# Performance work log

Hardware: AMD Instinct MI355X
Metric: run time of the kernel (lower is better)

Reference implementation:

```python
import jax, jax.numpy as jnp
import numpy as np

B, L, H, D = 4096, 256, 32, 2
LOG_PROB_FACTOR = 0.5

def setup_inputs() -> dict:
    key = jax.random.key(0)
    k0, k1, k2, k3 = jax.random.split(key, 4)
    x = jax.random.randint(k0, (B, L), 0, D)  # spin configs in {0,1}
    Wi = jax.random.normal(k1, (D, 4 * H), dtype=jnp.float32) * 0.1   # input kernel (no bias, flax LSTMCell)
    Wh = jax.random.normal(k2, (H, 4 * H), dtype=jnp.float32) * 0.1   # recurrent kernel
    bh = jnp.zeros((4 * H,), dtype=jnp.float32)                        # recurrent bias
    Wo = jax.random.normal(k3, (H, D), dtype=jnp.float32) * 0.1       # output Dense kernel
    bo = jnp.zeros((D,), dtype=jnp.float32)                            # output Dense bias
    return {"x": x, "Wi": Wi, "Wh": Wh, "bh": bh, "Wo": Wo, "bo": bo}

def reference(x, Wi, Wh, bh, Wo, bo):
    # one-hot of spin t-1 (zeros at t=0); log-prob is read out at spin t.
    x_oh = jax.nn.one_hot(x, D, dtype=Wi.dtype)      # [B, L, D]
    xs = jnp.swapaxes(x_oh, 0, 1)                    # [L, B, D] time-major for scan
    c0 = jnp.zeros((x.shape[0], H), Wi.dtype)
    h0 = jnp.zeros((x.shape[0], H), Wi.dtype)
    inp0 = jnp.zeros((x.shape[0], D), Wi.dtype)      # jnp.zeros(inputDim) initial input

    def step(carry, xt):
        c, h, inp = carry
        gates = inp @ Wi + h @ Wh + bh               # [B, 4H]
        i, f, g, o = jnp.split(gates, 4, axis=-1)    # flax LSTMCell gate order i,f,g,o
        c_new = jax.nn.sigmoid(f) * c + jax.nn.sigmoid(i) * jnp.tanh(g)
        h_new = jax.nn.sigmoid(o) * jnp.tanh(c_new)
        out = jax.nn.elu(h_new @ Wo + bo)            # Dense + actFun, [B, D]
        # log(sum(softmax(out) * onehot)) == gathered log_softmax (stable form)
        logp = jnp.sum(jax.nn.log_softmax(out, axis=-1) * xt, axis=-1)  # [B]
        return (c_new, h_new, xt), logp

    _, logps = jax.lax.scan(step, (c0, h0, inp0), xs)  # logps: [L, B]
    return LOG_PROB_FACTOR * jnp.sum(logps, axis=0)    # [B]
```

## Files before the change

kernel.cpp:

```cpp
#include <hip/hip_runtime.h>


typedef __attribute__((ext_vector_type(8))) short bf16x8;
typedef __attribute__((ext_vector_type(4))) float f32x4;

#define LOG2E 1.4426950408889634f
#define LN2   0.6931471805599453f

__device__ __forceinline__ float fexp2(float x) { return __builtin_amdgcn_exp2f(x); }
__device__ __forceinline__ float flog2(float x) { return __builtin_amdgcn_logf(x); }
__device__ __forceinline__ float frcp(float x)  { return __builtin_amdgcn_rcpf(x); }

__device__ __forceinline__ float fsig(float x)   { return frcp(1.f + fexp2(-LOG2E * x)); }
__device__ __forceinline__ float ftanh_(float x) { return 1.f - 2.f * frcp(fexp2(2.f * LOG2E * x) + 1.f); }
__device__ __forceinline__ float felu(float x)   { return x > 0.f ? x : fexp2(LOG2E * x) - 1.f; }

__device__ __forceinline__ unsigned short f2bf(float f) {
    unsigned u = __builtin_bit_cast(unsigned, f);
    u = (u + 0x7FFFu + ((u >> 16) & 1u)) >> 16;
    return (unsigned short)u;
}

__device__ __forceinline__ unsigned cvtpk_bf16(float a, float b) {
    unsigned r;
    asm("v_cvt_pk_bf16_f32 %0, %1, %2" : "=v"(r) : "v"(a), "v"(b));
    return r;
}

constexpr int Bsz = 4096;

__global__ __launch_bounds__(256, 1) void lstm_r19(
    const int*   __restrict__ x,
    const float* __restrict__ Wi,
    const float* __restrict__ Wh,
    const float* __restrict__ bh,
    const float* __restrict__ Wo,
    const float* __restrict__ bo,
    float*       __restrict__ out)
{
    const int tid  = threadIdx.x;
    const int w    = tid >> 6;
    const int lane = tid & 63;
    const int m    = lane & 15;
    const int oct  = lane >> 4;
    const int b0   = blockIdx.x * 16;

    extern __shared__ char dynpad[];
    __shared__ char   spinT[16][260];
    __shared__ float2 Sbuf[256][16];
    __shared__ short  hbuf[2][16][40];
    __shared__ float  red[16][16];
    if (blockIdx.x == 0xFFFFFFFFu) dynpad[0] = 1;

    {
        const int bl  = tid >> 4;
        const int c16 = (tid & 15) * 16;
        const int4* src = reinterpret_cast<const int4*>(x + (b0 + bl) * 256 + c16);
#pragma unroll
        for (int q = 0; q < 4; ++q) {
            const int4 v = src[q];
            const int pk = (v.x & 1) | ((v.y & 1) << 8) | ((v.z & 1) << 16) | ((v.w & 1) << 24);
            *reinterpret_cast<int*>(&spinT[bl][c16 + 4 * q]) = pk;
        }
    }

    bf16x8 wfrag[2];
    {
        const int r = m & 3;
        const float gs = (r == 2) ? 2.f * LOG2E : -LOG2E;
#pragma unroll
        for (int T = 0; T < 2; ++T) {
            const int colg = 32 * r + 8 * w + 2 * (m >> 2) + T;
#pragma unroll
            for (int j = 0; j < 8; ++j)
                wfrag[T][j] = (short)f2bf(gs * Wh[(8 * oct + j) * 128 + colg]);
        }
    }
    bf16x8 wfragO;
#pragma unroll
    for (int j = 0; j < 8; ++j)
        wfragO[j] = (m < 2) ? (short)f2bf(Wo[(8 * oct + j) * 2 + m]) : (short)0;

    const int uA = 8 * w + 2 * oct;
    const int uB = uA + 1;
    float bv0A[4], bvdA[4], bv0B[4], bvdB[4];
#pragma unroll
    for (int r = 0; r < 4; ++r) {
        const float gs = (r == 2) ? 2.f * LOG2E : -LOG2E;
        const int cA = 32 * r + uA, cB = 32 * r + uB;
        bv0A[r] = gs * (bh[cA] + Wi[cA]); bvdA[r] = gs * (Wi[128 + cA] - Wi[cA]);
        bv0B[r] = gs * (bh[cB] + Wi[cB]); bvdB[r] = gs * (Wi[128 + cB] - Wi[cB]);
    }
    const float bo0 = bo[0], bo1 = bo[1];

    float cA = fsig(bh[uA]) * ftanh_(bh[64 + uA]);
    float cB = fsig(bh[uB]) * ftanh_(bh[64 + uB]);
    {
        const float hA = fsig(bh[96 + uA]) * ftanh_(cA);
        const float hB = fsig(bh[96 + uB]) * ftanh_(cB);
        *reinterpret_cast<int*>(&hbuf[0][m][uA]) = (int)cvtpk_bf16(hA, hB);
    }
    __syncthreads();

    const f32x4 zero4 = { 0.f, 0.f, 0.f, 0.f };

    auto cellup = [](const f32x4 a, float& cc) -> float {
        const float ei = fexp2(a[0]), ef = fexp2(a[1]);
        const float eg = fexp2(a[2]), eo = fexp2(a[3]);
        const float P = (1.f + ei) * (1.f + eg);
        const float Q = 1.f + ef;
        const float R = frcp(P * Q);
        cc = fmaf(P * R, cc, (eg - 1.f) * Q * R);
        const float ec = fexp2(2.f * LOG2E * cc);
        return (ec - 1.f) * frcp((1.f + eo) * (1.f + ec));
    };

    auto step = [&](const int t, const int rb, const int wb,
                    const float spf, const int hw) {
        const bf16x8 hfrag =
            *reinterpret_cast<const bf16x8*>(&hbuf[rb][m][8 * oct]);

        f32x4 cbA, cbB;
#pragma unroll
        for (int r = 0; r < 4; ++r) {
            cbA[r] = fmaf(spf, bvdA[r], bv0A[r]);
            cbB[r] = fmaf(spf, bvdB[r], bv0B[r]);
        }

        const f32x4 accA = __builtin_amdgcn_mfma_f32_16x16x32_bf16(wfrag[0], hfrag, cbA, 0, 0, 0);
        const f32x4 accB = __builtin_amdgcn_mfma_f32_16x16x32_bf16(wfrag[1], hfrag, cbB, 0, 0, 0);

        if (w == hw) {
            const f32x4 aO = __builtin_amdgcn_mfma_f32_16x16x32_bf16(wfragO, hfrag, zero4, 0, 0, 0);
            if (oct == 0) Sbuf[t - 1][m] = make_float2(aO[0], aO[1]);
        }

        const float hA = cellup(accA, cA);
        const float hB = cellup(accB, cB);
        *reinterpret_cast<int*>(&hbuf[wb][m][uA]) = (int)cvtpk_bf16(hA, hB);
        __syncthreads();
    };

    unsigned sp4 = *reinterpret_cast<const unsigned*>(&spinT[m][0]);
    for (int tb = 1; tb < 253; tb += 4) {
        const unsigned sp4n =
            *reinterpret_cast<const unsigned*>(&spinT[m][tb + 3]);
        step(tb,     0, 1, (float)(sp4 & 0xFFu),         0);
        step(tb + 1, 1, 0, (float)((sp4 >> 8) & 0xFFu),  1);
        step(tb + 2, 0, 1, (float)((sp4 >> 16) & 0xFFu), 2);
        step(tb + 3, 1, 0, (float)(sp4 >> 24),           3);
        sp4 = sp4n;
    }
    step(253, 0, 1, (float)(sp4 & 0xFFu),         0);
    step(254, 1, 0, (float)((sp4 >> 8) & 0xFFu),  1);
    step(255, 0, 1, (float)((sp4 >> 16) & 0xFFu), 2);

    if (w == 3) {
        const bf16x8 hfrag = *reinterpret_cast<const bf16x8*>(&hbuf[1][m][8 * oct]);
        const f32x4 aO = __builtin_amdgcn_mfma_f32_16x16x32_bf16(wfragO, hfrag, zero4, 0, 0, 0);
        if (oct == 0) Sbuf[255][m] = make_float2(aO[0], aO[1]);
    }
    __syncthreads();

    float lp = 0.f;
    {
        const int bpost = tid & 15;
        const int tc    = tid >> 4;
#pragma unroll
        for (int i = 0; i < 16; ++i) {
            const int t = tc * 16 + i;
            const float2 sv = Sbuf[t][bpost];
            const int sp = spinT[bpost][t];
            const float o0 = felu(sv.x + bo0);
            const float o1 = felu(sv.y + bo1);
            const float mx = fmaxf(o0, o1), mn = fminf(o0, o1);
            const float lse = mx + LN2 * flog2(1.f + fexp2(LOG2E * (mn - mx)));
            lp += (sp ? o1 : o0) - lse;
        }
        red[tc][bpost] = lp;
    }
    __syncthreads();
    if (tid < 16) {
        float s = 0.f;
#pragma unroll
        for (int tc2 = 0; tc2 < 16; ++tc2) s += red[tc2][tid];
        out[b0 + tid] = 0.5f * s;
    }
}

extern "C" void kernel_launch(void* const* d_in, const int* in_sizes, int n_in,
                              void* d_out, int out_size, void* d_ws, size_t ws_size,
                              hipStream_t stream) {
    const int*   x  = (const int*)d_in[0];
    const float* Wi = (const float*)d_in[1];
    const float* Wh = (const float*)d_in[2];
    const float* bh = (const float*)d_in[3];
    const float* Wo = (const float*)d_in[4];
    const float* bo = (const float*)d_in[5];
    float* out = (float*)d_out;

    lstm_r19<<<dim3(Bsz / 16), dim3(256), 45056, stream>>>(x, Wi, Wh, bh, Wo, bo, out);
}
```

Before: 133.7 us.

## Split LSTM hidden units across eight waves with one MFMA per step

Doubles the block from four to eight waves, so each wave handles one hidden unit per lane group and issues a single gate MFMA per step instead of two. This halves the per-wave serial work on the recurrence critical path, in exchange for a barrier across more waves every step. The output-projection MFMA now rotates across all eight waves. The dynamic shared-memory padding that held the block to one per CU is removed, which may allow more blocks to be resident.

```diff
diff --git a/kernel.cpp b/kernel.cpp
--- a/kernel.cpp
+++ b/kernel.cpp
@@ -29,7 +29,7 @@
 
 constexpr int Bsz = 4096;
 
-__global__ __launch_bounds__(256, 1) void lstm_r19(
+__global__ __launch_bounds__(512, 1) void lstm_r20(
     const int*   __restrict__ x,
     const float* __restrict__ Wi,
     const float* __restrict__ Wh,
@@ -45,99 +45,80 @@
     const int oct  = lane >> 4;
     const int b0   = blockIdx.x * 16;
 
-    extern __shared__ char dynpad[];
     __shared__ char   spinT[16][260];
     __shared__ float2 Sbuf[256][16];
     __shared__ short  hbuf[2][16][40];
-    __shared__ float  red[16][16];
-    if (blockIdx.x == 0xFFFFFFFFu) dynpad[0] = 1;
+    __shared__ float  red[32][16];
 
     {
-        const int bl  = tid >> 4;
-        const int c16 = (tid & 15) * 16;
-        const int4* src = reinterpret_cast<const int4*>(x + (b0 + bl) * 256 + c16);
-#pragma unroll
-        for (int q = 0; q < 4; ++q) {
-            const int4 v = src[q];
-            const int pk = (v.x & 1) | ((v.y & 1) << 8) | ((v.z & 1) << 16) | ((v.w & 1) << 24);
-            *reinterpret_cast<int*>(&spinT[bl][c16 + 4 * q]) = pk;
-        }
+        const int bl = tid >> 5;
+        const int c8 = (tid & 31) * 8;
+        const int4* src = reinterpret_cast<const int4*>(x + (b0 + bl) * 256 + c8);
+        const int4 v0 = src[0], v1 = src[1];
+        const int p0 = (v0.x & 1) | ((v0.y & 1) << 8) | ((v0.z & 1) << 16) | ((v0.w & 1) << 24);
+        const int p1 = (v1.x & 1) | ((v1.y & 1) << 8) | ((v1.z & 1) << 16) | ((v1.w & 1) << 24);
+        *reinterpret_cast<int*>(&spinT[bl][c8])     = p0;
+        *reinterpret_cast<int*>(&spinT[bl][c8 + 4]) = p1;
     }
 
-    bf16x8 wfrag[2];
+    bf16x8 wfrag;
     {
         const int r = m & 3;
         const float gs = (r == 2) ? 2.f * LOG2E : -LOG2E;
+        const int colg = 32 * r + 4 * w + (m >> 2);
 #pragma unroll
-        for (int T = 0; T < 2; ++T) {
-            const int colg = 32 * r + 8 * w + 2 * (m >> 2) + T;
-#pragma unroll
-            for (int j = 0; j < 8; ++j)
-                wfrag[T][j] = (short)f2bf(gs * Wh[(8 * oct + j) * 128 + colg]);
-        }
+        for (int j = 0; j < 8; ++j)
+            wfrag[j] = (short)f2bf(gs * Wh[(8 * oct + j) * 128 + colg]);
     }
     bf16x8 wfragO;
 #pragma unroll
     for (int j = 0; j < 8; ++j)
         wfragO[j] = (m < 2) ? (short)f2bf(Wo[(8 * oct + j) * 2 + m]) : (short)0;
 
-    const int uA = 8 * w + 2 * oct;
-    const int uB = uA + 1;
-    float bv0A[4], bvdA[4], bv0B[4], bvdB[4];
+    const int u = 4 * w + oct;
+    float bv0[4], bvd[4];
 #pragma unroll
     for (int r = 0; r < 4; ++r) {
         const float gs = (r == 2) ? 2.f * LOG2E : -LOG2E;
-        const int cA = 32 * r + uA, cB = 32 * r + uB;
-        bv0A[r] = gs * (bh[cA] + Wi[cA]); bvdA[r] = gs * (Wi[128 + cA] - Wi[cA]);
-        bv0B[r] = gs * (bh[cB] + Wi[cB]); bvdB[r] = gs * (Wi[128 + cB] - Wi[cB]);
+        const int c0 = 32 * r + u;
+        bv0[r] = gs * (bh[c0] + Wi[c0]);
+        bvd[r] = gs * (Wi[128 + c0] - Wi[c0]);
     }
     const float bo0 = bo[0], bo1 = bo[1];
 
-    float cA = fsig(bh[uA]) * ftanh_(bh[64 + uA]);
-    float cB = fsig(bh[uB]) * ftanh_(bh[64 + uB]);
-    {
-        const float hA = fsig(bh[96 + uA]) * ftanh_(cA);
-        const float hB = fsig(bh[96 + uB]) * ftanh_(cB);
-        *reinterpret_cast<int*>(&hbuf[0][m][uA]) = (int)cvtpk_bf16(hA, hB);
-    }
+    float c = fsig(bh[u]) * ftanh_(bh[64 + u]);
+    hbuf[0][m][u] = (short)f2bf(fsig(bh[96 + u]) * ftanh_(c));
     __syncthreads();
 
+    const int wS = __builtin_amdgcn_readfirstlane(w);
     const f32x4 zero4 = { 0.f, 0.f, 0.f, 0.f };
 
-    auto cellup = [](const f32x4 a, float& cc) -> float {
-        const float ei = fexp2(a[0]), ef = fexp2(a[1]);
-        const float eg = fexp2(a[2]), eo = fexp2(a[3]);
+    auto step = [&](const int t, const int rb, const int wb, const float spf) {
+        const bf16x8 hfrag =
+            *reinterpret_cast<const bf16x8*>(&hbuf[rb][m][8 * oct]);
+
+        f32x4 cb;
+#pragma unroll
+        for (int r = 0; r < 4; ++r) cb[r] = fmaf(spf, bvd[r], bv0[r]);
+
+        const f32x4 acc =
+            __builtin_amdgcn_mfma_f32_16x16x32_bf16(wfrag, hfrag, cb, 0, 0, 0);
+
+        const float ei = fexp2(acc[0]), ef = fexp2(acc[1]);
+        const float eg = fexp2(acc[2]), eo = fexp2(acc[3]);
         const float P = (1.f + ei) * (1.f + eg);
         const float Q = 1.f + ef;
         const float R = frcp(P * Q);
-        cc = fmaf(P * R, cc, (eg - 1.f) * Q * R);
-        const float ec = fexp2(2.f * LOG2E * cc);
-        return (ec - 1.f) * frcp((1.f + eo) * (1.f + ec));
-    };
+        c = fmaf(P * R, c, (eg - 1.f) * Q * R);
+        const float ec = fexp2(2.f * LOG2E * c);
+        const float h  = (ec - 1.f) * frcp((1.f + eo) * (1.f + ec));
+        hbuf[wb][m][u] = (short)cvtpk_bf16(h, h);
 
-    auto step = [&](const int t, const int rb, const int wb,
-                    const float spf, const int hw) {
-        const bf16x8 hfrag =
-            *reinterpret_cast<const bf16x8*>(&hbuf[rb][m][8 * oct]);
-
-        f32x4 cbA, cbB;
-#pragma unroll
-        for (int r = 0; r < 4; ++r) {
-            cbA[r] = fmaf(spf, bvdA[r], bv0A[r]);
-            cbB[r] = fmaf(spf, bvdB[r], bv0B[r]);
-        }
-
-        const f32x4 accA = __builtin_amdgcn_mfma_f32_16x16x32_bf16(wfrag[0], hfrag, cbA, 0, 0, 0);
-        const f32x4 accB = __builtin_amdgcn_mfma_f32_16x16x32_bf16(wfrag[1], hfrag, cbB, 0, 0, 0);
-
-        if (w == hw) {
-            const f32x4 aO = __builtin_amdgcn_mfma_f32_16x16x32_bf16(wfragO, hfrag, zero4, 0, 0, 0);
+        if (wS == ((t - 1) & 7)) {
+            const f32x4 aO =
+                __builtin_amdgcn_mfma_f32_16x16x32_bf16(wfragO, hfrag, zero4, 0, 0, 0);
             if (oct == 0) Sbuf[t - 1][m] = make_float2(aO[0], aO[1]);
         }
-
-        const float hA = cellup(accA, cA);
-        const float hB = cellup(accB, cB);
-        *reinterpret_cast<int*>(&hbuf[wb][m][uA]) = (int)cvtpk_bf16(hA, hB);
         __syncthreads();
     };
 
@@ -145,19 +126,20 @@
     for (int tb = 1; tb < 253; tb += 4) {
         const unsigned sp4n =
             *reinterpret_cast<const unsigned*>(&spinT[m][tb + 3]);
-        step(tb,     0, 1, (float)(sp4 & 0xFFu),         0);
-        step(tb + 1, 1, 0, (float)((sp4 >> 8) & 0xFFu),  1);
-        step(tb + 2, 0, 1, (float)((sp4 >> 16) & 0xFFu), 2);
-        step(tb + 3, 1, 0, (float)(sp4 >> 24),           3);
+        step(tb,     0, 1, (float)(sp4 & 0xFFu));
+        step(tb + 1, 1, 0, (float)((sp4 >> 8) & 0xFFu));
+        step(tb + 2, 0, 1, (float)((sp4 >> 16) & 0xFFu));
+        step(tb + 3, 1, 0, (float)(sp4 >> 24));
         sp4 = sp4n;
     }
-    step(253, 0, 1, (float)(sp4 & 0xFFu),         0);
-    step(254, 1, 0, (float)((sp4 >> 8) & 0xFFu),  1);
-    step(255, 0, 1, (float)((sp4 >> 16) & 0xFFu), 2);
+    step(253, 0, 1, (float)(sp4 & 0xFFu));
+    step(254, 1, 0, (float)((sp4 >> 8) & 0xFFu));
+    step(255, 0, 1, (float)((sp4 >> 16) & 0xFFu));
 
-    if (w == 3) {
+    if (wS == 7) {
         const bf16x8 hfrag = *reinterpret_cast<const bf16x8*>(&hbuf[1][m][8 * oct]);
-        const f32x4 aO = __builtin_amdgcn_mfma_f32_16x16x32_bf16(wfragO, hfrag, zero4, 0, 0, 0);
+        const f32x4 aO =
+            __builtin_amdgcn_mfma_f32_16x16x32_bf16(wfragO, hfrag, zero4, 0, 0, 0);
         if (oct == 0) Sbuf[255][m] = make_float2(aO[0], aO[1]);
     }
     __syncthreads();
@@ -167,8 +149,8 @@
         const int bpost = tid & 15;
         const int tc    = tid >> 4;
 #pragma unroll
-        for (int i = 0; i < 16; ++i) {
-            const int t = tc * 16 + i;
+        for (int i = 0; i < 8; ++i) {
+            const int t = tc * 8 + i;
             const float2 sv = Sbuf[t][bpost];
             const int sp = spinT[bpost][t];
             const float o0 = felu(sv.x + bo0);
@@ -183,7 +165,7 @@
     if (tid < 16) {
         float s = 0.f;
 #pragma unroll
-        for (int tc2 = 0; tc2 < 16; ++tc2) s += red[tc2][tid];
+        for (int tc2 = 0; tc2 < 32; ++tc2) s += red[tc2][tid];
         out[b0 + tid] = 0.5f * s;
     }
 }
@@ -199,5 +181,5 @@
     const float* bo = (const float*)d_in[5];
     float* out = (float*)d_out;
 
-    lstm_r19<<<dim3(Bsz / 16), dim3(256), 45056, stream>>>(x, Wi, Wh, bh, Wo, bo, out);
+    lstm_r20<<<dim3(Bsz / 16), dim3(512), 0, stream>>>(x, Wi, Wh, bh, Wo, bo, out);
 }
```

Result: faster. 120.6 us (-9.7%).
